# Kernel tuning notes

Measured on AMD Instinct MI355X. Metric: run time of the kernel, lower is better.

Reference implementation:

```python
import jax, jax.numpy as jnp
import numpy as np

SEQ, BS, H, I, E = 2048, 4, 2048, 4096, 8


def setup_inputs() -> dict:
    key = jax.random.key(0)
    ks = jax.random.split(key, 5)
    s = 0.02
    return {
        "hidden_states": jax.random.normal(ks[0], (SEQ, BS, H), dtype=jnp.float32),
        "router_w": jax.random.normal(ks[1], (H, E), dtype=jnp.float32) * s,
        "gate_w": jax.random.normal(ks[2], (E, H, I), dtype=jnp.float32) * s,
        "up_w": jax.random.normal(ks[3], (E, H, I), dtype=jnp.float32) * s,
        "down_w": jax.random.normal(ks[4], (E, I, H), dtype=jnp.float32) * s,
    }


def reference(hidden_states, router_w, gate_w, up_w, down_w):
    # Router: [S,B,H] @ [H,E] -> [S,B,E]; top-1 routing (num_experts_per_tok == 1)
    router_logits = jnp.einsum("sbh,he->sbe", hidden_states, router_w)
    routing_indices = jnp.argmax(router_logits, axis=-1)  # [S,B]
    # sigmoid routing weights are computed but NOT applied in the original combine
    routing_weights = jax.nn.sigmoid(jnp.max(router_logits, axis=-1))  # noqa: F841

    out = jnp.zeros_like(hidden_states)
    for e in range(E):  # small fixed expert count
        mask = (routing_indices == e)[..., None]  # [S,B,1]
        g = jnp.einsum("sbh,hi->sbi", hidden_states, gate_w[e])
        u = jnp.einsum("sbh,hi->sbi", hidden_states, up_w[e])
        y = jnp.einsum("sbi,ih->sbh", jax.nn.silu(g) * u, down_w[e])
        out = out + jnp.where(mask, y, jnp.zeros((), out.dtype))
    return out
```

## Files before the change

### kernel.cpp

```cpp
#include <hip/hip_runtime.h>
#include <hip/hip_bf16.h>

#define T_TOKENS 8192
#define H_DIM 2048
#define I_DIM 4096
#define E_EXP 8
#define PAD_ROWS 9216

typedef __bf16 bf16x8 __attribute__((ext_vector_type(8)));
typedef float floatx4 __attribute__((ext_vector_type(4)));
typedef unsigned short ushort8 __attribute__((ext_vector_type(8)));

__device__ __forceinline__ unsigned short f2bf(float f) {
  union { float f; unsigned int i; } c; c.f = f;
  unsigned int x = c.i;
  unsigned int r = x + 0x7fffu + ((x >> 16) & 1u);
  return (unsigned short)(r >> 16);
}

__device__ __forceinline__ float bf2float(unsigned short u) {
  union { unsigned int i; float f; } c; c.i = ((unsigned int)u) << 16;
  return c.f;
}

__device__ __forceinline__ void gload_lds16(const void* g, void* l) {
  __builtin_amdgcn_global_load_lds(
      (const __attribute__((address_space(1))) void*)g,
      (__attribute__((address_space(3))) void*)l, 16, 0, 0);
}

__device__ __forceinline__ void cvt_slab(const float* __restrict__ W,
                                         unsigned short* __restrict__ Wt,
                                         int K, int N, int e, int kg, int nb,
                                         int tid) {
  const int n0 = tid * 4;
  const float* src = W + (size_t)e * K * N + (size_t)kg * 8 * N + nb + n0;
  unsigned short* dst = Wt + (size_t)e * K * N
                        + ((size_t)kg * (N >> 4) + (nb >> 4)) * 128;
  floatx4 a[8];
#pragma unroll
  for (int kk = 0; kk < 8; ++kk)
    a[kk] = __builtin_nontemporal_load((const floatx4*)(src + (size_t)kk * N));
#pragma unroll
  for (int nn = 0; nn < 4; ++nn) {
    const int n = n0 + nn;
    ushort8 o;
#pragma unroll
    for (int kk = 0; kk < 8; ++kk) o[kk] = f2bf(a[kk][nn]);
    *(ushort8*)(dst + (size_t)(n >> 4) * 128 + (n & 15) * 8) = o;
  }
}

__global__ __launch_bounds__(256) void router_cvt_kernel(
    const float* __restrict__ x, const float* __restrict__ rw,
    const float* __restrict__ gw, const float* __restrict__ uw,
    unsigned short* __restrict__ xb, int* __restrict__ idx,
    int* __restrict__ hdr, unsigned short* __restrict__ Wg,
    unsigned short* __restrict__ Wu) {
  if (blockIdx.x >= 2048) {
    int bid = blockIdx.x - 2048;
    const float* W = (bid < 8192) ? gw : uw;
    unsigned short* Wt = (bid < 8192) ? Wg : Wu;
    bid &= 8191;
    const int e = bid >> 10;
    const int rem = bid & 1023;
    cvt_slab(W, Wt, H_DIM, I_DIM, e, rem >> 2, (rem & 3) * 1024, threadIdx.x);
    return;
  }
  const int lane = threadIdx.x & 63;
  const int t = blockIdx.x * 4 + (threadIdx.x >> 6);
  const float* xr = x + (size_t)t * H_DIM;
  unsigned short* xbr = xb + (size_t)t * H_DIM;
  float acc[8];
#pragma unroll
  for (int e = 0; e < 8; ++e) acc[e] = 0.f;
#pragma unroll
  for (int j = 0; j < 8; ++j) {
    const int c0 = (lane + j * 64) * 4;
    floatx4 v = *(const floatx4*)(xr + c0);
    ushort4 o;
    o.x = f2bf(v[0]); o.y = f2bf(v[1]); o.z = f2bf(v[2]); o.w = f2bf(v[3]);
    *(ushort4*)(xbr + c0) = o;
#pragma unroll
    for (int cc = 0; cc < 4; ++cc) {
      const float h = v[cc];
      floatx4 r0 = *(const floatx4*)(rw + (size_t)(c0 + cc) * 8);
      floatx4 r1 = *(const floatx4*)(rw + (size_t)(c0 + cc) * 8 + 4);
#pragma unroll
      for (int e = 0; e < 4; ++e) { acc[e] += h * r0[e]; acc[e + 4] += h * r1[e]; }
    }
  }
#pragma unroll
  for (int off = 32; off > 0; off >>= 1)
#pragma unroll
    for (int e = 0; e < 8; ++e) acc[e] += __shfl_xor(acc[e], off, 64);
  if (lane == 0) {
    int best = 0; float bv = acc[0];
#pragma unroll
    for (int e = 1; e < 8; ++e) if (acc[e] > bv) { bv = acc[e]; best = e; }
    idx[t] = best;
    atomicAdd(&hdr[best], 1);
  }
}

__global__ __launch_bounds__(256) void setup_kernel(int* __restrict__ hdr,
                                                    int* __restrict__ rows) {
  if (threadIdx.x == 0) {
    int b = 0;
    for (int e = 0; e < 8; ++e) {
      hdr[16 + e] = b;
      b += ((hdr[e] + 127) >> 7) << 7;
    }
  }
  for (int i = threadIdx.x; i < PAD_ROWS; i += 256) rows[i] = -1;
}

__global__ __launch_bounds__(256) void scatter_kernel(const int* __restrict__ idx,
                                                      int* __restrict__ hdr,
                                                      int* __restrict__ rows) {
  int t = blockIdx.x * 256 + threadIdx.x;
  int e = idx[t];
  int p = atomicAdd(&hdr[8 + e], 1);
  rows[hdr[16 + e] + p] = t;
}

__global__ __launch_bounds__(256) void cvt_down_kernel(const float* __restrict__ W,
                                                       unsigned short* __restrict__ Wt) {
  const int bid = blockIdx.x;
  const int e = bid >> 10;
  const int rem = bid & 1023;
  cvt_slab(W, Wt, I_DIM, H_DIM, e, rem >> 1, (rem & 1) * 1024, threadIdx.x);
}

__global__ __launch_bounds__(256, 2) void moe_gemm_gu(
    const unsigned short* __restrict__ A,
    const unsigned short* __restrict__ Bg,
    const unsigned short* __restrict__ Bu,
    const int* __restrict__ hdr,
    const int* __restrict__ rows,
    unsigned short* __restrict__ inter,
    const float* __restrict__ dw,
    unsigned short* __restrict__ Wd) {
  if (blockIdx.y >= 64) {
    const int cid = (((int)blockIdx.y - 64) * 32 + (int)blockIdx.x) * 8 + (int)blockIdx.z;
    const int e = cid >> 10;
    const int rem = cid & 1023;
    cvt_slab(dw, Wd, I_DIM, H_DIM, e, rem >> 1, (rem & 1) * 1024, threadIdx.x);
    return;
  }
  const int e = blockIdx.z;
  const int cnt = hdr[e];
  if ((int)blockIdx.y * 128 >= cnt) return;
  const int seg = hdr[16 + e];

  const int tid = threadIdx.x;
  const int lane = tid & 63;
  const int wv = tid >> 6;
  const int wm = (wv & 1) * 64;
  const int wn = (wv >> 1) * 64;
  const int q = lane >> 4;
  const int l15 = lane & 15;

  __shared__ unsigned short sA[128 * 64];
  __shared__ unsigned short sBg[64 * 128];
  __shared__ unsigned short sBu[64 * 128];

  const int lr = lane >> 3;
  const int colsw = (lane & 7) ^ lr;
  const unsigned short* aptr[4];
#pragma unroll
  for (int j = 0; j < 4; ++j) {
    const int R = j * 32 + wv * 8 + lr;
    int ar = rows[seg + blockIdx.y * 128 + R];
    if (ar < 0) ar = 0;
    aptr[j] = A + (size_t)ar * H_DIM + colsw * 8;
  }

  const int N16 = I_DIM / 16;
  const int ng0 = blockIdx.x * 8;
  const unsigned short* BgE = Bg + (size_t)e * I_DIM * H_DIM;
  const unsigned short* BuE = Bu + (size_t)e * I_DIM * H_DIM;

  floatx4 accg[4][4], accu[4][4];
#pragma unroll
  for (int a = 0; a < 4; ++a)
#pragma unroll
    for (int b = 0; b < 4; ++b) {
      accg[a][b] = (floatx4){0.f, 0.f, 0.f, 0.f};
      accu[a][b] = (floatx4){0.f, 0.f, 0.f, 0.f};
    }

  const int ubB = q * 1024 + l15 * 8;
  const int wn16o = (wn >> 4) * 128;

  for (int kt = 0; kt < H_DIM; kt += 64) {
#pragma unroll
    for (int j = 0; j < 4; ++j) {
      gload_lds16(aptr[j] + kt, sA + (j * 32 + wv * 8) * 64);
      const int g = j * 4 + wv;
      const int kgg = (kt >> 3) + (g >> 1);
      const size_t so = (size_t)(kgg * N16 + ng0 + (g & 1) * 4) * 128 + lane * 8;
      gload_lds16(BgE + so, sBg + g * 512);
      gload_lds16(BuE + so, sBu + g * 512);
    }
    __syncthreads();
#pragma unroll
    for (int ks = 0; ks < 64; ks += 32) {
      const int sbase = ks >> 3;
      const int bbase = ks * 128 + wn16o + ubB;
      bf16x8 af[4], bfr[4];
#pragma unroll
      for (int fm = 0; fm < 4; ++fm) {
        const int ra = wm + fm * 16 + l15;
        af[fm] = __builtin_bit_cast(bf16x8,
            *(const ushort8*)(sA + ra * 64 + (((q + sbase) ^ (ra & 7)) << 3)));
      }
#pragma unroll
      for (int fn = 0; fn < 4; ++fn)
        bfr[fn] = __builtin_bit_cast(bf16x8,
            *(const ushort8*)(sBg + bbase + fn * 128));
#pragma unroll
      for (int fm = 0; fm < 4; ++fm)
#pragma unroll
        for (int fn = 0; fn < 4; ++fn)
          accg[fm][fn] = __builtin_amdgcn_mfma_f32_16x16x32_bf16(af[fm], bfr[fn],
                                                                 accg[fm][fn], 0, 0, 0);
#pragma unroll
      for (int fn = 0; fn < 4; ++fn)
        bfr[fn] = __builtin_bit_cast(bf16x8,
            *(const ushort8*)(sBu + bbase + fn * 128));
#pragma unroll
      for (int fm = 0; fm < 4; ++fm)
#pragma unroll
        for (int fn = 0; fn < 4; ++fn)
          accu[fm][fn] = __builtin_amdgcn_mfma_f32_16x16x32_bf16(af[fm], bfr[fn],
                                                                 accu[fm][fn], 0, 0, 0);
    }
    __syncthreads();
  }

#pragma unroll
  for (int fm = 0; fm < 4; ++fm)
#pragma unroll
    for (int fn = 0; fn < 4; ++fn)
#pragma unroll
      for (int rr = 0; rr < 4; ++rr) {
        const int row = wm + fm * 16 + q * 4 + rr;
        const int col = wn + fn * 16 + l15;
        const int gm = blockIdx.y * 128 + row;
        const int gn = blockIdx.x * 128 + col;
        const float g = accg[fm][fn][rr];
        const float u = accu[fm][fn][rr];
        const float s = g / (1.f + __expf(-g));
        inter[(size_t)(seg + gm) * I_DIM + gn] = f2bf(s * u);
      }
}

__global__ __launch_bounds__(256, 2) void moe_gemm_down(
    const unsigned short* __restrict__ A,
    const unsigned short* __restrict__ Bt,
    const int* __restrict__ hdr,
    const int* __restrict__ rows,
    float* __restrict__ outp) {
  const int e = blockIdx.z;
  const int cnt = hdr[e];
  if ((int)blockIdx.y * 128 >= cnt) return;
  const int seg = hdr[16 + e];

  const int tid = threadIdx.x;
  const int lane = tid & 63;
  const int wv = tid >> 6;
  const int wm = (wv & 1) * 64;
  const int wn = (wv >> 1) * 64;
  const int q = lane >> 4;
  const int l15 = lane & 15;

  __shared__ unsigned short sA[128 * 64];
  __shared__ unsigned short sB0[64 * 128];
  __shared__ unsigned short sB1[64 * 128];

  const int lr = lane >> 3;
  const int colsw = (lane & 7) ^ lr;
  const unsigned short* aptr[4];
#pragma unroll
  for (int j = 0; j < 4; ++j) {
    const int R = j * 32 + wv * 8 + lr;
    aptr[j] = A + (size_t)(seg + blockIdx.y * 128 + R) * I_DIM + colsw * 8;
  }

  const int N16 = H_DIM / 16;
  const int ng0 = blockIdx.x * 16;
  const unsigned short* Be = Bt + (size_t)e * H_DIM * I_DIM;

  floatx4 acc0[4][4], acc1[4][4];
#pragma unroll
  for (int a = 0; a < 4; ++a)
#pragma unroll
    for (int b = 0; b < 4; ++b) {
      acc0[a][b] = (floatx4){0.f, 0.f, 0.f, 0.f};
      acc1[a][b] = (floatx4){0.f, 0.f, 0.f, 0.f};
    }

  const int ubB = q * 1024 + l15 * 8;
  const int wn16o = (wn >> 4) * 128;

  for (int kt = 0; kt < I_DIM; kt += 64) {
#pragma unroll
    for (int j = 0; j < 4; ++j) {
      gload_lds16(aptr[j] + kt, sA + (j * 32 + wv * 8) * 64);
      const int g = j * 4 + wv;
      const int kgg = (kt >> 3) + (g >> 1);
      const size_t so0 = (size_t)(kgg * N16 + ng0 + (g & 1) * 4) * 128 + lane * 8;
      const size_t so1 = (size_t)(kgg * N16 + ng0 + 8 + (g & 1) * 4) * 128 + lane * 8;
      gload_lds16(Be + so0, sB0 + g * 512);
      gload_lds16(Be + so1, sB1 + g * 512);
    }
    __syncthreads();
#pragma unroll
    for (int ks = 0; ks < 64; ks += 32) {
      const int sbase = ks >> 3;
      const int bbase = ks * 128 + wn16o + ubB;
      bf16x8 af[4], bfr[4];
#pragma unroll
      for (int fm = 0; fm < 4; ++fm) {
        const int ra = wm + fm * 16 + l15;
        af[fm] = __builtin_bit_cast(bf16x8,
            *(const ushort8*)(sA + ra * 64 + (((q + sbase) ^ (ra & 7)) << 3)));
      }
#pragma unroll
      for (int fn = 0; fn < 4; ++fn)
        bfr[fn] = __builtin_bit_cast(bf16x8,
            *(const ushort8*)(sB0 + bbase + fn * 128));
#pragma unroll
      for (int fm = 0; fm < 4; ++fm)
#pragma unroll
        for (int fn = 0; fn < 4; ++fn)
          acc0[fm][fn] = __builtin_amdgcn_mfma_f32_16x16x32_bf16(af[fm], bfr[fn],
                                                                 acc0[fm][fn], 0, 0, 0);
#pragma unroll
      for (int fn = 0; fn < 4; ++fn)
        bfr[fn] = __builtin_bit_cast(bf16x8,
            *(const ushort8*)(sB1 + bbase + fn * 128));
#pragma unroll
      for (int fm = 0; fm < 4; ++fm)
#pragma unroll
        for (int fn = 0; fn < 4; ++fn)
          acc1[fm][fn] = __builtin_amdgcn_mfma_f32_16x16x32_bf16(af[fm], bfr[fn],
                                                                 acc1[fm][fn], 0, 0, 0);
    }
    __syncthreads();
  }

#pragma unroll
  for (int fm = 0; fm < 4; ++fm)
#pragma unroll
    for (int rr = 0; rr < 4; ++rr) {
      const int row = wm + fm * 16 + q * 4 + rr;
      const int tok = rows[seg + blockIdx.y * 128 + row];
      if (tok < 0) continue;
      float* orow = outp + (size_t)tok * H_DIM + blockIdx.x * 256;
#pragma unroll
      for (int fn = 0; fn < 4; ++fn) {
        const int col = wn + fn * 16 + l15;
        orow[col]       = acc0[fm][fn][rr];
        orow[128 + col] = acc1[fm][fn][rr];
      }
    }
}

extern "C" void kernel_launch(void* const* d_in, const int* in_sizes, int n_in,
                              void* d_out, int out_size, void* d_ws, size_t ws_size,
                              hipStream_t stream) {
  const float* hidden   = (const float*)d_in[0];
  const float* router_w = (const float*)d_in[1];
  const float* gate_w   = (const float*)d_in[2];
  const float* up_w     = (const float*)d_in[3];
  const float* down_w   = (const float*)d_in[4];
  float* out = (float*)d_out;

  char* ws = (char*)d_ws;
  int* hdr  = (int*)ws;
  int* idx  = (int*)(ws + 1024);
  int* rows = (int*)(ws + 33792);
  unsigned short* x_bf  = (unsigned short*)(ws + 70656);
  unsigned short* inter = (unsigned short*)(ws + 33625088);
  unsigned short* W1    = (unsigned short*)(ws + 109122560);
  unsigned short* W2    = (unsigned short*)(ws + 243340288);
  unsigned short* W3    = (unsigned short*)(ws + 377558016);
  const bool big = ws_size >= 511775744ull;

  hipMemsetAsync(hdr, 0, 128, stream);
  router_cvt_kernel<<<2048 + 16384, 256, 0, stream>>>(
      hidden, router_w, gate_w, up_w, x_bf, idx, hdr, W1, W2);
  setup_kernel<<<1, 256, 0, stream>>>(hdr, rows);
  scatter_kernel<<<T_TOKENS / 256, 256, 0, stream>>>(idx, hdr, rows);

  if (big) {
    moe_gemm_gu<<<dim3(I_DIM / 128, 96, E_EXP), 256, 0, stream>>>(
        x_bf, W1, W2, hdr, rows, inter, down_w, W3);
    moe_gemm_down<<<dim3(H_DIM / 256, 64, E_EXP), 256, 0, stream>>>(
        inter, W3, hdr, rows, out);
  } else {
    moe_gemm_gu<<<dim3(I_DIM / 128, 64, E_EXP), 256, 0, stream>>>(
        x_bf, W1, W2, hdr, rows, inter, nullptr, nullptr);
    cvt_down_kernel<<<8192, 256, 0, stream>>>(down_w, W1);
    moe_gemm_down<<<dim3(H_DIM / 256, 64, E_EXP), 256, 0, stream>>>(
        inter, W1, hdr, rows, out);
  }
}
```

Measured before the change: 1.447 ms.

## Split-K the down-projection GEMM into two halves with a separate add-scatter pass

Splits the K dimension (I) of the down-projection grouped GEMM into two halves, doubling the number of workgroups so that more CUs have work. Each half writes fp32 partials to workspace buffers that reuse the W1/W2 region. A new add_scatter kernel sums the two partials and scatters rows to their token positions. This buys more parallelism at the cost of writing and reading two fp32 partial buffers plus an extra launch. It applies only to the large-workspace path.

```diff
diff --git a/kernel.cpp b/kernel.cpp
--- a/kernel.cpp
+++ b/kernel.cpp
@@ -16,11 +16,6 @@
   unsigned int x = c.i;
   unsigned int r = x + 0x7fffu + ((x >> 16) & 1u);
   return (unsigned short)(r >> 16);
-}
-
-__device__ __forceinline__ float bf2float(unsigned short u) {
-  union { unsigned int i; float f; } c; c.i = ((unsigned int)u) << 16;
-  return c.f;
 }
 
 __device__ __forceinline__ void gload_lds16(const void* g, void* l) {
@@ -256,6 +251,136 @@
       }
 }
 
+__global__ __launch_bounds__(256, 2) void moe_gemm_down_sk(
+    const unsigned short* __restrict__ A,
+    const unsigned short* __restrict__ Bt,
+    const int* __restrict__ hdr,
+    float* __restrict__ p0,
+    float* __restrict__ p1) {
+  const int e = blockIdx.z;
+  const int cnt = hdr[e];
+  const int ytile = blockIdx.y >> 1;
+  const int khalf = blockIdx.y & 1;
+  if (ytile * 128 >= cnt) return;
+  const int seg = hdr[16 + e];
+
+  const int tid = threadIdx.x;
+  const int lane = tid & 63;
+  const int wv = tid >> 6;
+  const int wm = (wv & 1) * 64;
+  const int wn = (wv >> 1) * 64;
+  const int q = lane >> 4;
+  const int l15 = lane & 15;
+
+  __shared__ unsigned short sA[128 * 64];
+  __shared__ unsigned short sB0[64 * 128];
+  __shared__ unsigned short sB1[64 * 128];
+
+  const int lr = lane >> 3;
+  const int colsw = (lane & 7) ^ lr;
+  const unsigned short* aptr[4];
+#pragma unroll
+  for (int j = 0; j < 4; ++j) {
+    const int R = j * 32 + wv * 8 + lr;
+    aptr[j] = A + (size_t)(seg + ytile * 128 + R) * I_DIM + colsw * 8;
+  }
+
+  const int N16 = H_DIM / 16;
+  const int ng0 = blockIdx.x * 16;
+  const unsigned short* Be = Bt + (size_t)e * H_DIM * I_DIM;
+
+  floatx4 acc0[4][4], acc1[4][4];
+#pragma unroll
+  for (int a = 0; a < 4; ++a)
+#pragma unroll
+    for (int b = 0; b < 4; ++b) {
+      acc0[a][b] = (floatx4){0.f, 0.f, 0.f, 0.f};
+      acc1[a][b] = (floatx4){0.f, 0.f, 0.f, 0.f};
+    }
+
+  const int ubB = q * 1024 + l15 * 8;
+  const int wn16o = (wn >> 4) * 128;
+  const int k0 = khalf * (I_DIM / 2);
+
+  for (int kt = k0; kt < k0 + I_DIM / 2; kt += 64) {
+#pragma unroll
+    for (int j = 0; j < 4; ++j) {
+      gload_lds16(aptr[j] + kt, sA + (j * 32 + wv * 8) * 64);
+      const int g = j * 4 + wv;
+      const int kgg = (kt >> 3) + (g >> 1);
+      const size_t so0 = (size_t)(kgg * N16 + ng0 + (g & 1) * 4) * 128 + lane * 8;
+      const size_t so1 = (size_t)(kgg * N16 + ng0 + 8 + (g & 1) * 4) * 128 + lane * 8;
+      gload_lds16(Be + so0, sB0 + g * 512);
+      gload_lds16(Be + so1, sB1 + g * 512);
+    }
+    __syncthreads();
+#pragma unroll
+    for (int ks = 0; ks < 64; ks += 32) {
+      const int sbase = ks >> 3;
+      const int bbase = ks * 128 + wn16o + ubB;
+      bf16x8 af[4], bfr[4];
+#pragma unroll
+      for (int fm = 0; fm < 4; ++fm) {
+        const int ra = wm + fm * 16 + l15;
+        af[fm] = __builtin_bit_cast(bf16x8,
+            *(const ushort8*)(sA + ra * 64 + (((q + sbase) ^ (ra & 7)) << 3)));
+      }
+#pragma unroll
+      for (int fn = 0; fn < 4; ++fn)
+        bfr[fn] = __builtin_bit_cast(bf16x8,
+            *(const ushort8*)(sB0 + bbase + fn * 128));
+#pragma unroll
+      for (int fm = 0; fm < 4; ++fm)
+#pragma unroll
+        for (int fn = 0; fn < 4; ++fn)
+          acc0[fm][fn] = __builtin_amdgcn_mfma_f32_16x16x32_bf16(af[fm], bfr[fn],
+                                                                 acc0[fm][fn], 0, 0, 0);
+#pragma unroll
+      for (int fn = 0; fn < 4; ++fn)
+        bfr[fn] = __builtin_bit_cast(bf16x8,
+            *(const ushort8*)(sB1 + bbase + fn * 128));
+#pragma unroll
+      for (int fm = 0; fm < 4; ++fm)
+#pragma unroll
+        for (int fn = 0; fn < 4; ++fn)
+          acc1[fm][fn] = __builtin_amdgcn_mfma_f32_16x16x32_bf16(af[fm], bfr[fn],
+                                                                 acc1[fm][fn], 0, 0, 0);
+    }
+    __syncthreads();
+  }
+
+  float* pp = khalf ? p1 : p0;
+#pragma unroll
+  for (int fm = 0; fm < 4; ++fm)
+#pragma unroll
+    for (int rr = 0; rr < 4; ++rr) {
+      const int row = wm + fm * 16 + q * 4 + rr;
+      float* orow = pp + (size_t)(seg + ytile * 128 + row) * H_DIM + blockIdx.x * 256;
+#pragma unroll
+      for (int fn = 0; fn < 4; ++fn) {
+        const int col = wn + fn * 16 + l15;
+        orow[col]       = acc0[fm][fn][rr];
+        orow[128 + col] = acc1[fm][fn][rr];
+      }
+    }
+}
+
+__global__ __launch_bounds__(256) void add_scatter_kernel(
+    const float* __restrict__ p0, const float* __restrict__ p1,
+    const int* __restrict__ rows, float* __restrict__ outp) {
+  const int r = blockIdx.x;
+  const int tok = rows[r];
+  if (tok < 0) return;
+  const floatx4* a = (const floatx4*)(p0 + (size_t)r * H_DIM);
+  const floatx4* b = (const floatx4*)(p1 + (size_t)r * H_DIM);
+  floatx4* o = (floatx4*)(outp + (size_t)tok * H_DIM);
+#pragma unroll
+  for (int i = 0; i < 2; ++i) {
+    const int c = i * 256 + threadIdx.x;
+    o[c] = a[c] + b[c];
+  }
+}
+
 __global__ __launch_bounds__(256, 2) void moe_gemm_down(
     const unsigned short* __restrict__ A,
     const unsigned short* __restrict__ Bt,
@@ -387,6 +512,8 @@
   unsigned short* W1    = (unsigned short*)(ws + 109122560);
   unsigned short* W2    = (unsigned short*)(ws + 243340288);
   unsigned short* W3    = (unsigned short*)(ws + 377558016);
+  float* p0 = (float*)W1;
+  float* p1 = (float*)(ws + 109122560 + 75497472);
   const bool big = ws_size >= 511775744ull;
 
   hipMemsetAsync(hdr, 0, 128, stream);
@@ -398,8 +525,9 @@
   if (big) {
     moe_gemm_gu<<<dim3(I_DIM / 128, 96, E_EXP), 256, 0, stream>>>(
         x_bf, W1, W2, hdr, rows, inter, down_w, W3);
-    moe_gemm_down<<<dim3(H_DIM / 256, 64, E_EXP), 256, 0, stream>>>(
-        inter, W3, hdr, rows, out);
+    moe_gemm_down_sk<<<dim3(H_DIM / 256, 128, E_EXP), 256, 0, stream>>>(
+        inter, W3, hdr, p0, p1);
+    add_scatter_kernel<<<PAD_ROWS, 256, 0, stream>>>(p0, p1, rows, out);
   } else {
     moe_gemm_gu<<<dim3(I_DIM / 128, 64, E_EXP), 256, 0, stream>>>(
         x_bf, W1, W2, hdr, rows, inter, nullptr, nullptr);
```

New measurement: 1.435 ms. Within noise of the previous version (-0.8%).
